# Kernel tuning notes

Measured on AMD Instinct MI355X. Metric: run time of the kernel, lower is better.

Reference implementation:

```python
import jax, jax.numpy as jnp
import numpy as np

B, S, E, H = 4, 2048, 1024, 16
D = E // H  # head dim = 64
NEG = -1e9


def setup_inputs() -> dict:
    key = jax.random.key(0)
    ks = jax.random.split(key, 6)
    scale = 1.0 / np.sqrt(E)
    return {
        "x": jax.random.normal(ks[0], (B, S, E), dtype=jnp.float32),
        "in_proj_weight": jax.random.normal(ks[1], (3 * E, E), dtype=jnp.float32) * scale,
        "in_proj_bias": jax.random.normal(ks[2], (3 * E,), dtype=jnp.float32) * 0.02,
        "out_proj_weight": jax.random.normal(ks[3], (E, E), dtype=jnp.float32) * scale,
        "out_proj_bias": jax.random.normal(ks[4], (E,), dtype=jnp.float32) * 0.02,
        "mask": jax.random.randint(ks[5], (B, S), 0, 2, dtype=jnp.int32),
    }


def reference(x, in_proj_weight, in_proj_bias, out_proj_weight, out_proj_bias, mask):
    # Equivalent of F.multi_head_attention_forward(h,h,h,...) with batch-first x.
    # qkv projection: [B,S,3E]
    qkv = jnp.einsum("bse,fe->bsf", x, in_proj_weight) + in_proj_bias
    q, k, v = jnp.split(qkv, 3, axis=-1)
    # split heads -> [B,S,H,D]
    q = q.reshape(B, S, H, D) * (1.0 / np.sqrt(D))
    k = k.reshape(B, S, H, D)
    v = v.reshape(B, S, H, D)
    # scores [B,H,Sq,Sk]
    scores = jnp.einsum("bqhd,bkhd->bhqk", q, k)
    # key_padding_mask = (mask == 0): True positions are excluded
    pad = (mask == 0)[:, None, None, :]  # [B,1,1,Sk]
    scores = jnp.where(pad, NEG, scores)
    attn = jax.nn.softmax(scores, axis=-1)
    # attention output -> [B,S,E]
    ctx = jnp.einsum("bhqk,bkhd->bqhd", attn, v).reshape(B, S, E)
    h_ = jnp.einsum("bse,fe->bsf", ctx, out_proj_weight) + out_proj_bias
    # residual; dropout is identity in eval mode
    return x + h_
```

## Files before the change

kernel.cpp:

```cpp
#include <hip/hip_runtime.h>
#include <stdint.h>
#include <math.h>

#define B_ 4
#define S_ 2048
#define E_ 1024
#define H_ 16
#define D_ 64
#define M_ (B_*S_)

typedef __attribute__((ext_vector_type(8))) short bf16x8;
typedef __attribute__((ext_vector_type(4))) float f32x4;

__device__ __forceinline__ unsigned short f2bf(float f) {
  union { float f; uint32_t u; } v; v.f = f;
  uint32_t u = v.u;
  return (unsigned short)((u + 0x7FFFu + ((u >> 16) & 1u)) >> 16);
}

__device__ __forceinline__ void gload16(const void* g, void* l) {
  __builtin_amdgcn_global_load_lds(
      (__attribute__((address_space(1))) void*)g,
      (__attribute__((address_space(3))) void*)l, 16, 0, 0);
}

__device__ __forceinline__ uint32_t cvtpk(float lo, float hi) {
  uint32_t r;
  asm("v_cvt_pk_bf16_f32 %0, %1, %2" : "=v"(r) : "v"(lo), "v"(hi));
  return r;
}

#define N1 ((M_*E_)/4)
#define N2 ((3*E_*E_)/4)
#define N3 ((E_*E_)/4)
#define NM ((B_*S_)/4)
__global__ __launch_bounds__(256) void cvt_all(const float* __restrict__ x,
                                               const float* __restrict__ w1,
                                               const float* __restrict__ w2,
                                               const int* __restrict__ mask,
                                               unsigned short* __restrict__ dst,
                                               float* __restrict__ maskf) {
  int i = blockIdx.x * 256 + threadIdx.x;
  if (i < N1 + N2 + N3) {
    const float* src;
    int j;
    if (i < N1) { src = x; j = i; }
    else if (i < N1 + N2) { src = w1; j = i - N1; }
    else { src = w2; j = i - N1 - N2; }
    float4 v = reinterpret_cast<const float4*>(src)[j];
    ushort4 o;
    o.x = f2bf(v.x); o.y = f2bf(v.y); o.z = f2bf(v.z); o.w = f2bf(v.w);
    reinterpret_cast<ushort4*>(dst)[i] = o;
  } else if (i < N1 + N2 + N3 + NM) {
    int j = i - (N1 + N2 + N3);
    int4 m = reinterpret_cast<const int4*>(mask)[j];
    float4 o;
    o.x = m.x ? 0.0f : -2.0e9f;
    o.y = m.y ? 0.0f : -2.0e9f;
    o.z = m.z ? 0.0f : -2.0e9f;
    o.w = m.w ? 0.0f : -2.0e9f;
    reinterpret_cast<float4*>(maskf)[j] = o;
  }
}

__device__ __forceinline__ void stage_half(const unsigned short* src,
                                           unsigned short* dst, int tid, int o0) {
  gload16(src + o0, dst + tid * 8);
  gload16(src + o0 + 65536, dst + tid * 8 + 4096);
}

template<int Q, int W>
__device__ __forceinline__ void phase256(
    const unsigned short* At, const unsigned short* Bt,
    bf16x8 (&bfm)[4][2], f32x4 (&acc)[8][4],
    const unsigned short* ssrc, unsigned short* sdst,
    int tid, int o0, int wm, int wn, int l15, int lg)
{
  bf16x8 afr[2][2];
  if constexpr (Q == 0) {
    const unsigned short* bh = Bt + (wn >> 1) * 8192;
    #pragma unroll
    for (int nf = 0; nf < 4; ++nf) {
      const int rowB = (wn & 1) * 64 + nf * 16 + l15;
      #pragma unroll
      for (int ks = 0; ks < 2; ++ks)
        bfm[nf][ks] = *(const bf16x8*)&bh[rowB * 64 + (((ks*4 + lg) ^ (rowB & 7)) * 8)];
    }
  }
  const unsigned short* ah = At + wm * 8192;
  #pragma unroll
  for (int sub = 0; sub < 2; ++sub) {
    const int rowA = (2*Q + sub) * 16 + l15;
    #pragma unroll
    for (int ks = 0; ks < 2; ++ks)
      afr[sub][ks] = *(const bf16x8*)&ah[rowA * 64 + (((ks*4 + lg) ^ (rowA & 7)) * 8)];
  }
  if (ssrc) stage_half(ssrc, sdst, tid, o0);
  if constexpr (W == 2) asm volatile("s_waitcnt vmcnt(2)" ::: "memory");
  if constexpr (W == 4) asm volatile("s_waitcnt vmcnt(4)" ::: "memory");
  if constexpr (W == 9) asm volatile("s_waitcnt vmcnt(0)" ::: "memory");
  asm volatile("" ::: "memory");
  __builtin_amdgcn_s_barrier();
  asm volatile("s_waitcnt lgkmcnt(0)" ::: "memory");
  __builtin_amdgcn_sched_barrier(0);
  __builtin_amdgcn_s_setprio(1);
  #pragma unroll
  for (int sub = 0; sub < 2; ++sub)
    #pragma unroll
    for (int nf = 0; nf < 4; ++nf)
      #pragma unroll
      for (int ks = 0; ks < 2; ++ks)
        acc[2*Q + sub][nf] = __builtin_amdgcn_mfma_f32_16x16x32_bf16(
            afr[sub][ks], bfm[nf][ks], acc[2*Q + sub][nf], 0, 0, 0);
  __builtin_amdgcn_s_setprio(0);
  asm volatile("" ::: "memory");
  __builtin_amdgcn_s_barrier();
  asm volatile("" ::: "memory");
}

__global__ __launch_bounds__(512, 2) void gemm_qkv8(
    const unsigned short* __restrict__ A,
    const unsigned short* __restrict__ W,
    const float* __restrict__ bias,
    unsigned short* __restrict__ Qg,
    unsigned short* __restrict__ Kg,
    unsigned short* __restrict__ Vtg)
{
  __shared__ __align__(16) unsigned short AsF[2 * 16384];
  __shared__ __align__(16) unsigned short BsF[2 * 16384];
  const int tid = threadIdx.x;
  const int lane = tid & 63, wave = tid >> 6;
  const int wm = wave >> 2, wn = wave & 3;
  const int l15 = lane & 15, lg = lane >> 4;

  int lin = blockIdx.y * 12 + blockIdx.x;
  lin = (lin & 7) * 48 + (lin >> 3);
  const int tm = (lin / 12) * 256;
  const int tn = (lin % 12) * 256;

  const int o0 = (tid >> 3) * 1024 + (((tid & 7) ^ ((tid >> 3) & 7)) * 8);
  const unsigned short* Ab = A + (size_t)tm * 1024;
  const unsigned short* Bb = W + (size_t)tn * 1024;

#define SRCA(t,h) (Ab + (size_t)((t)*64 + (h)*131072))
#define SRCB(t,h) (Bb + (size_t)((t)*64 + (h)*131072))
#define DSTA(b,h) (AsF + (b)*16384 + (h)*8192)
#define DSTB(b,h) (BsF + (b)*16384 + (h)*8192)

  f32x4 acc[8][4];
  #pragma unroll
  for (int mi = 0; mi < 8; ++mi)
    #pragma unroll
    for (int nf = 0; nf < 4; ++nf) acc[mi][nf] = (f32x4){0.f, 0.f, 0.f, 0.f};
  bf16x8 bfm[4][2];

  stage_half(SRCA(0,0), DSTA(0,0), tid, o0);
  stage_half(SRCA(0,1), DSTA(0,1), tid, o0);
  stage_half(SRCB(0,0), DSTB(0,0), tid, o0);
  stage_half(SRCB(0,1), DSTB(0,1), tid, o0);
  stage_half(SRCB(1,0), DSTB(1,0), tid, o0);
  stage_half(SRCB(1,1), DSTB(1,1), tid, o0);
  asm volatile("s_waitcnt vmcnt(4)" ::: "memory");
  __builtin_amdgcn_s_barrier();
  asm volatile("" ::: "memory");

  for (int i = 0; i < 7; ++i) {
    const int t2 = 2 * i;
    const unsigned short* A0t = DSTA(0,0);
    const unsigned short* B0t = DSTB(0,0);
    const unsigned short* A1t = DSTA(1,0);
    const unsigned short* B1t = DSTB(1,0);
    phase256<0,0>(A0t, B0t, bfm, acc, SRCA(t2+1,0), DSTA(1,0), tid, o0, wm, wn, l15, lg);
    phase256<1,0>(A0t, B0t, bfm, acc, SRCB(t2+2,0), DSTB(0,0), tid, o0, wm, wn, l15, lg);
    phase256<2,0>(A0t, B0t, bfm, acc, SRCB(t2+2,1), DSTB(0,1), tid, o0, wm, wn, l15, lg);
    phase256<3,0>(A0t, B0t, bfm, acc, SRCA(t2+1,1), DSTA(1,1), tid, o0, wm, wn, l15, lg);
    phase256<0,2>(A1t, B1t, bfm, acc, SRCA(t2+2,0), DSTA(0,0), tid, o0, wm, wn, l15, lg);
    phase256<1,0>(A1t, B1t, bfm, acc, SRCA(t2+2,1), DSTA(0,1), tid, o0, wm, wn, l15, lg);
    phase256<2,0>(A1t, B1t, bfm, acc, SRCB(t2+3,0), DSTB(1,0), tid, o0, wm, wn, l15, lg);
    phase256<3,4>(A1t, B1t, bfm, acc, SRCB(t2+3,1), DSTB(1,1), tid, o0, wm, wn, l15, lg);
  }
  {
    const unsigned short* A0t = DSTA(0,0);
    const unsigned short* B0t = DSTB(0,0);
    const unsigned short* A1t = DSTA(1,0);
    const unsigned short* B1t = DSTB(1,0);
    phase256<0,0>(A0t, B0t, bfm, acc, SRCA(15,0), DSTA(1,0), tid, o0, wm, wn, l15, lg);
    phase256<1,0>(A0t, B0t, bfm, acc, nullptr, nullptr, tid, o0, wm, wn, l15, lg);
    phase256<2,0>(A0t, B0t, bfm, acc, nullptr, nullptr, tid, o0, wm, wn, l15, lg);
    phase256<3,0>(A0t, B0t, bfm, acc, SRCA(15,1), DSTA(1,1), tid, o0, wm, wn, l15, lg);
    phase256<0,9>(A1t, B1t, bfm, acc, nullptr, nullptr, tid, o0, wm, wn, l15, lg);
    phase256<1,0>(A1t, B1t, bfm, acc, nullptr, nullptr, tid, o0, wm, wn, l15, lg);
    phase256<2,0>(A1t, B1t, bfm, acc, nullptr, nullptr, tid, o0, wm, wn, l15, lg);
    phase256<3,0>(A1t, B1t, bfm, acc, nullptr, nullptr, tid, o0, wm, wn, l15, lg);
  }
#undef SRCA
#undef SRCB
#undef DSTA
#undef DSTB

  #pragma unroll
  for (int nf = 0; nf < 4; ++nf) {
    const int col = tn + wn * 64 + nf * 16 + l15;
    const float bcol = bias[col];
    const int sec = col >> 10;
    const int f2 = col & 1023;
    const int h = f2 >> 6, d = f2 & 63;
    #pragma unroll
    for (int mi = 0; mi < 8; ++mi) {
      #pragma unroll
      for (int r = 0; r < 4; ++r) {
        const int row = tm + wm * 128 + mi * 16 + lg * 4 + r;
        const int b = row >> 11, s = row & (S_-1);
        const size_t bh = (size_t)(b * H_ + h);
        float val = acc[mi][nf][r] + bcol;
        if (sec == 0) {
          Qg[(bh*S_ + s)*D_ + d] = f2bf(val * 0.18033688f);
        } else if (sec == 1) {
          const int ch = (d >> 3) ^ (s & 7);
          Kg[(bh*S_ + s)*D_ + ch*8 + (d & 7)] = f2bf(val);
        } else {
          const int c2 = ((s >> 3) & 7) ^ (d & 7);
          Vtg[(bh*D_ + d)*S_ + (s & ~63) + c2*8 + (s & 7)] = f2bf(val);
        }
      }
    }
  }
}

__global__ __launch_bounds__(512, 4) void attn_fwd(
    const unsigned short* __restrict__ Qg,
    const unsigned short* __restrict__ Kg,
    const unsigned short* __restrict__ Vtg,
    const float* __restrict__ maskf,
    unsigned short* __restrict__ ctx)
{
  __shared__ __align__(16) unsigned short Ks[2][4096];
  __shared__ __align__(16) unsigned short Vs[2][4096];
  const int tid = threadIdx.x, lane = tid & 63, wave = tid >> 6;
  const int l15 = lane & 15, lg = lane >> 4;
  const int bh = blockIdx.y, b = bh >> 4, h = bh & 15;
  const int q0 = blockIdx.x * 256 + wave * 32;
  const unsigned short* Qb = Qg + (size_t)bh * S_ * D_;
  const unsigned short* Kb = Kg + (size_t)bh * S_ * D_;
  const unsigned short* Vb = Vtg + (size_t)bh * D_ * S_;
  const float* mrow = maskf + b * S_;

  bf16x8 qf[2][2];
  #pragma unroll
  for (int mi = 0; mi < 2; ++mi)
    #pragma unroll
    for (int kc = 0; kc < 2; ++kc)
      qf[mi][kc] = *(const bf16x8*)&Qb[(size_t)(q0 + mi*16 + l15)*D_ + kc*32 + lg*8];

  f32x4 zero4 = {0.f, 0.f, 0.f, 0.f};
  f32x4 accO[2][4];
  f32x4 accL[2] = {zero4, zero4};
  #pragma unroll
  for (int mi = 0; mi < 2; ++mi)
    #pragma unroll
    for (int df = 0; df < 4; ++df) accO[mi][df] = zero4;

  union { uint32_t u[4]; bf16x8 v; } ou;
  ou.u[0] = ou.u[1] = ou.u[2] = ou.u[3] = 0x3F803F80u;
  const bf16x8 onesv = ou.v;

  int kboff0[4], kboff1[4], vboff0[4], vboff1[4];
  #pragma unroll
  for (int kt = 0; kt < 4; ++kt) {
    const int krow = kt*16 + l15;
    kboff0[kt] = (krow*64 + ((lg ^ (krow & 7))*8)) * 2;
    kboff1[kt] = (krow*64 + (((4+lg) ^ (krow & 7))*8)) * 2;
  }
  #pragma unroll
  for (int df = 0; df < 4; ++df) {
    const int vrow = df*16 + l15;
    vboff0[df] = (vrow*64 + ((lg ^ (vrow & 7))*8)) * 2;
    vboff1[df] = (vrow*64 + (((4+lg) ^ (vrow & 7))*8)) * 2;
  }
  const char* KsB = (const char*)&Ks[0][0];
  const char* VsB = (const char*)&Vs[0][0];

  const int sr0 = tid >> 3, sc0 = (tid & 7) * 8;

  gload16(Kb + (size_t)sr0 * D_ + sc0, &Ks[0][tid*8]);
  gload16(Vb + (size_t)sr0 * S_ + sc0, &Vs[0][tid*8]);
  f32x4 mv0[4], mv1[4];
  #pragma unroll
  for (int kt = 0; kt < 4; ++kt)
    mv0[kt] = *(const f32x4*)&mrow[kt*16 + lg*4];
  const unsigned short* kpre = Kb + (size_t)(64 + sr0) * D_ + sc0;
  const unsigned short* vpre = Vb + (size_t)sr0 * S_ + 64 + sc0;
  const float* mpre = mrow + 64 + lg*4;
  __syncthreads();

#define ATTN_TILE(CUR, MVC, MVN, DO_PF)                                         \
  {                                                                             \
    if (DO_PF) {                                                                \
      gload16(kpre, &Ks[(CUR)^1][tid*8]);                                       \
      gload16(vpre, &Vs[(CUR)^1][tid*8]);                                       \
      kpre += 64*D_; vpre += 64;                                                \
      _Pragma("unroll")                                                         \
      for (int kt = 0; kt < 4; ++kt)                                            \
        MVN[kt] = *(const f32x4*)&mpre[kt*16];                                  \
      mpre += 64;                                                               \
    }                                                                           \
    f32x4 s_[2][4];                                                             \
    __builtin_amdgcn_s_setprio(1);                                              \
    _Pragma("unroll")                                                           \
    for (int kt = 0; kt < 4; ++kt) {                                            \
      bf16x8 kf0 = *(const bf16x8*)(KsB + (CUR)*8192 + kboff0[kt]);             \
      bf16x8 kf1 = *(const bf16x8*)(KsB + (CUR)*8192 + kboff1[kt]);             \
      s_[0][kt] = __builtin_amdgcn_mfma_f32_16x16x32_bf16(kf0, qf[0][0], MVC[kt], 0, 0, 0); \
      s_[0][kt] = __builtin_amdgcn_mfma_f32_16x16x32_bf16(kf1, qf[0][1], s_[0][kt], 0, 0, 0); \
      s_[1][kt] = __builtin_amdgcn_mfma_f32_16x16x32_bf16(kf0, qf[1][0], MVC[kt], 0, 0, 0); \
      s_[1][kt] = __builtin_amdgcn_mfma_f32_16x16x32_bf16(kf1, qf[1][1], s_[1][kt], 0, 0, 0); \
    }                                                                           \
    __builtin_amdgcn_s_setprio(0);                                              \
    _Pragma("unroll")                                                           \
    for (int mi = 0; mi < 2; ++mi)                                              \
      _Pragma("unroll")                                                         \
      for (int kt = 0; kt < 4; ++kt)                                            \
        _Pragma("unroll")                                                       \
        for (int r = 0; r < 4; ++r)                                             \
          s_[mi][kt][r] = __builtin_amdgcn_exp2f(s_[mi][kt][r]);                \
    bf16x8 pa[2][2];                                                            \
    _Pragma("unroll")                                                           \
    for (int mi = 0; mi < 2; ++mi) {                                            \
      _Pragma("unroll")                                                         \
      for (int kk = 0; kk < 2; ++kk) {                                          \
        uint32_t a0 = cvtpk(s_[mi][2*kk][0],   s_[mi][2*kk][1]);                \
        uint32_t c1 = cvtpk(s_[mi][2*kk][2],   s_[mi][2*kk][3]);                \
        uint32_t b0 = cvtpk(s_[mi][2*kk+1][0], s_[mi][2*kk+1][1]);              \
        uint32_t d1 = cvtpk(s_[mi][2*kk+1][2], s_[mi][2*kk+1][3]);              \
        asm("v_permlane32_swap_b32 %0, %1" : "+v"(a0), "+v"(b0));               \
        asm("v_permlane16_swap_b32 %0, %1" : "+v"(a0), "+v"(b0));               \
        asm("v_permlane32_swap_b32 %0, %1" : "+v"(c1), "+v"(d1));               \
        asm("v_permlane16_swap_b32 %0, %1" : "+v"(c1), "+v"(d1));               \
        union { bf16x8 v; uint32_t u[4]; } w;                                   \
        w.u[0] = a0; w.u[1] = c1; w.u[2] = b0; w.u[3] = d1;                     \
        pa[mi][kk] = w.v;                                                       \
      }                                                                         \
    }                                                                           \
    __builtin_amdgcn_s_setprio(1);                                              \
    accL[0] = __builtin_amdgcn_mfma_f32_16x16x32_bf16(pa[0][0], onesv, accL[0], 0, 0, 0); \
    accL[1] = __builtin_amdgcn_mfma_f32_16x16x32_bf16(pa[1][0], onesv, accL[1], 0, 0, 0); \
    _Pragma("unroll")                                                           \
    for (int df = 0; df < 4; ++df) {                                            \
      bf16x8 vf = *(const bf16x8*)(VsB + (CUR)*8192 + vboff0[df]);              \
      accO[0][df] = __builtin_amdgcn_mfma_f32_16x16x32_bf16(pa[0][0], vf, accO[0][df], 0, 0, 0); \
      accO[1][df] = __builtin_amdgcn_mfma_f32_16x16x32_bf16(pa[1][0], vf, accO[1][df], 0, 0, 0); \
    }                                                                           \
    accL[0] = __builtin_amdgcn_mfma_f32_16x16x32_bf16(pa[0][1], onesv, accL[0], 0, 0, 0); \
    accL[1] = __builtin_amdgcn_mfma_f32_16x16x32_bf16(pa[1][1], onesv, accL[1], 0, 0, 0); \
    _Pragma("unroll")                                                           \
    for (int df = 0; df < 4; ++df) {                                            \
      bf16x8 vf = *(const bf16x8*)(VsB + (CUR)*8192 + vboff1[df]);              \
      accO[0][df] = __builtin_amdgcn_mfma_f32_16x16x32_bf16(pa[0][1], vf, accO[0][df], 0, 0, 0); \
      accO[1][df] = __builtin_amdgcn_mfma_f32_16x16x32_bf16(pa[1][1], vf, accO[1][df], 0, 0, 0); \
    }                                                                           \
    __builtin_amdgcn_s_setprio(0);                                              \
    __syncthreads();                                                            \
  }

  for (int tt = 0; tt < 32; tt += 2) {
    ATTN_TILE(0, mv0, mv1, 1)
    ATTN_TILE(1, mv1, mv0, (tt < 30))
  }
#undef ATTN_TILE

  #pragma unroll
  for (int mi = 0; mi < 2; ++mi) {
    #pragma unroll
    for (int r = 0; r < 4; ++r) {
      const float iv = 1.0f / accL[mi][r];
      const int srow = q0 + mi*16 + lg*4 + r;
      #pragma unroll
      for (int df = 0; df < 4; ++df) {
        const int d = df*16 + l15;
        ctx[((size_t)b*S_ + srow)*E_ + h*D_ + d] = f2bf(accO[mi][df][r] * iv);
      }
    }
  }
}

__global__ __launch_bounds__(256) void gemm_out(
    const unsigned short* __restrict__ A,
    const unsigned short* __restrict__ W,
    const float* __restrict__ bias,
    const float* __restrict__ xres,
    float* __restrict__ out)
{
  __shared__ __align__(16) unsigned short As[128*32];
  __shared__ __align__(16) unsigned short Bs[128*32];
  const int tid = threadIdx.x;
  const int lane = tid & 63;
  const int wave = tid >> 6;
  const int wm = (wave >> 1) * 64, wn = (wave & 1) * 64;
  const int tm = blockIdx.y * 128, tn = blockIdx.x * 128;
  const int l15 = lane & 15, lg = lane >> 4;

  f32x4 zero4 = {0.f, 0.f, 0.f, 0.f};
  f32x4 acc[4][4];
  #pragma unroll
  for (int mi = 0; mi < 4; ++mi)
    #pragma unroll
    for (int ni = 0; ni < 4; ++ni) acc[mi][ni] = zero4;

  const int r0 = tid >> 2, c0 = (tid & 3) * 8;
  const unsigned short* Arow0 = A + (size_t)(tm + r0) * E_ + c0;
  const unsigned short* Arow1 = A + (size_t)(tm + r0 + 64) * E_ + c0;
  const unsigned short* Wrow0 = W + (size_t)(tn + r0) * E_ + c0;
  const unsigned short* Wrow1 = W + (size_t)(tn + r0 + 64) * E_ + c0;
  unsigned short* lA0 = As + tid * 8;
  unsigned short* lA1 = As + (tid + 256) * 8;
  unsigned short* lB0 = Bs + tid * 8;
  unsigned short* lB1 = Bs + (tid + 256) * 8;

  for (int k0 = 0; k0 < E_; k0 += 32) {
    gload16(Arow0 + k0, lA0);
    gload16(Arow1 + k0, lA1);
    gload16(Wrow0 + k0, lB0);
    gload16(Wrow1 + k0, lB1);
    __syncthreads();
    bf16x8 af[4], bfm[4];
    #pragma unroll
    for (int mi = 0; mi < 4; ++mi)
      af[mi] = *(const bf16x8*)&As[(wm + mi*16 + l15)*32 + lg*8];
    #pragma unroll
    for (int ni = 0; ni < 4; ++ni)
      bfm[ni] = *(const bf16x8*)&Bs[(wn + ni*16 + l15)*32 + lg*8];
    #pragma unroll
    for (int mi = 0; mi < 4; ++mi)
      #pragma unroll
      for (int ni = 0; ni < 4; ++ni)
        acc[mi][ni] = __builtin_amdgcn_mfma_f32_16x16x32_bf16(af[mi], bfm[ni], acc[mi][ni], 0, 0, 0);
    __syncthreads();
  }

  #pragma unroll
  for (int ni = 0; ni < 4; ++ni) {
    const int col = tn + wn + ni*16 + l15;
    const float bcol = bias[col];
    #pragma unroll
    for (int mi = 0; mi < 4; ++mi) {
      #pragma unroll
      for (int r = 0; r < 4; ++r) {
        const int row = tm + wm + mi*16 + lg*4 + r;
        out[(size_t)row*E_ + col] = xres[(size_t)row*E_ + col] + acc[mi][ni][r] + bcol;
      }
    }
  }
}

extern "C" void kernel_launch(void* const* d_in, const int* in_sizes, int n_in,
                              void* d_out, int out_size, void* d_ws, size_t ws_size,
                              hipStream_t stream) {
  const float* x  = (const float*)d_in[0];
  const float* w1 = (const float*)d_in[1];
  const float* b1 = (const float*)d_in[2];
  const float* w2 = (const float*)d_in[3];
  const float* b2 = (const float*)d_in[4];
  const int* mask = (const int*)d_in[5];
  float* out = (float*)d_out;

  const size_t SZ = (size_t)B_*H_*S_*D_;
  unsigned short* Qg  = (unsigned short*)d_ws;
  unsigned short* Kg  = Qg + SZ;
  unsigned short* Vtg = Kg + SZ;
  unsigned short* xb  = Vtg + SZ;
  unsigned short* w1b = xb + (size_t)M_*E_;
  unsigned short* w2b = w1b + (size_t)3*E_*E_;
  float* maskf = (float*)(w2b + (size_t)E_*E_);
  unsigned short* ctx = xb;

  const int ntot = N1 + N2 + N3 + NM;
  cvt_all<<<(ntot + 255)/256, 256, 0, stream>>>(x, w1, w2, mask, xb, maskf);

  gemm_qkv8<<<dim3(12, 32), 512, 0, stream>>>(xb, w1b, b1, Qg, Kg, Vtg);
  attn_fwd<<<dim3(S_/256, B_*H_), 512, 0, stream>>>(Qg, Kg, Vtg, maskf, ctx);
  gemm_out<<<dim3(E_/128, M_/128), 256, 0, stream>>>(ctx, w2b, b2, x, out);
}
```

Baseline: 231.0 us.

## Replace pipelined 256x256 QKV GEMM with simple 128x128 tile and LDS-transposed V store

Swaps the double-buffered, phase-scheduled 256x256 QKV projection kernel for a simpler 128x128 tile kernel. The new kernel uses 256 threads, a 32-wide K step and two __syncthreads per iteration, and remaps blocks so each XCD works on contiguous column tiles. The V section now goes through an LDS transpose so it can write the transposed, swizzled V with 16-byte coalesced stores instead of scattered 2-byte stores. The intent is more blocks for occupancy and better V store efficiency. In exchange it loses the load/compute overlap, the LDS swizzle and the larger per-block reuse, so the GEMM may become latency bound with bank conflicts.

```diff
diff --git a/kernel.cpp b/kernel.cpp
--- a/kernel.cpp
+++ b/kernel.cpp
@@ -63,62 +63,7 @@
   }
 }
 
-__device__ __forceinline__ void stage_half(const unsigned short* src,
-                                           unsigned short* dst, int tid, int o0) {
-  gload16(src + o0, dst + tid * 8);
-  gload16(src + o0 + 65536, dst + tid * 8 + 4096);
-}
-
-template<int Q, int W>
-__device__ __forceinline__ void phase256(
-    const unsigned short* At, const unsigned short* Bt,
-    bf16x8 (&bfm)[4][2], f32x4 (&acc)[8][4],
-    const unsigned short* ssrc, unsigned short* sdst,
-    int tid, int o0, int wm, int wn, int l15, int lg)
-{
-  bf16x8 afr[2][2];
-  if constexpr (Q == 0) {
-    const unsigned short* bh = Bt + (wn >> 1) * 8192;
-    #pragma unroll
-    for (int nf = 0; nf < 4; ++nf) {
-      const int rowB = (wn & 1) * 64 + nf * 16 + l15;
-      #pragma unroll
-      for (int ks = 0; ks < 2; ++ks)
-        bfm[nf][ks] = *(const bf16x8*)&bh[rowB * 64 + (((ks*4 + lg) ^ (rowB & 7)) * 8)];
-    }
-  }
-  const unsigned short* ah = At + wm * 8192;
-  #pragma unroll
-  for (int sub = 0; sub < 2; ++sub) {
-    const int rowA = (2*Q + sub) * 16 + l15;
-    #pragma unroll
-    for (int ks = 0; ks < 2; ++ks)
-      afr[sub][ks] = *(const bf16x8*)&ah[rowA * 64 + (((ks*4 + lg) ^ (rowA & 7)) * 8)];
-  }
-  if (ssrc) stage_half(ssrc, sdst, tid, o0);
-  if constexpr (W == 2) asm volatile("s_waitcnt vmcnt(2)" ::: "memory");
-  if constexpr (W == 4) asm volatile("s_waitcnt vmcnt(4)" ::: "memory");
-  if constexpr (W == 9) asm volatile("s_waitcnt vmcnt(0)" ::: "memory");
-  asm volatile("" ::: "memory");
-  __builtin_amdgcn_s_barrier();
-  asm volatile("s_waitcnt lgkmcnt(0)" ::: "memory");
-  __builtin_amdgcn_sched_barrier(0);
-  __builtin_amdgcn_s_setprio(1);
-  #pragma unroll
-  for (int sub = 0; sub < 2; ++sub)
-    #pragma unroll
-    for (int nf = 0; nf < 4; ++nf)
-      #pragma unroll
-      for (int ks = 0; ks < 2; ++ks)
-        acc[2*Q + sub][nf] = __builtin_amdgcn_mfma_f32_16x16x32_bf16(
-            afr[sub][ks], bfm[nf][ks], acc[2*Q + sub][nf], 0, 0, 0);
-  __builtin_amdgcn_s_setprio(0);
-  asm volatile("" ::: "memory");
-  __builtin_amdgcn_s_barrier();
-  asm volatile("" ::: "memory");
-}
-
-__global__ __launch_bounds__(512, 2) void gemm_qkv8(
+__global__ __launch_bounds__(256) void gemm_qkv128(
     const unsigned short* __restrict__ A,
     const unsigned short* __restrict__ W,
     const float* __restrict__ bias,
@@ -126,103 +71,113 @@
     unsigned short* __restrict__ Kg,
     unsigned short* __restrict__ Vtg)
 {
-  __shared__ __align__(16) unsigned short AsF[2 * 16384];
-  __shared__ __align__(16) unsigned short BsF[2 * 16384];
+  __shared__ __align__(16) unsigned short SMEM[128*136];
+  unsigned short* As = SMEM;
+  unsigned short* Bs = SMEM + 4096;
   const int tid = threadIdx.x;
-  const int lane = tid & 63, wave = tid >> 6;
-  const int wm = wave >> 2, wn = wave & 3;
+  const int lane = tid & 63;
+  const int wave = tid >> 6;
+  const int wm = (wave >> 1) * 64, wn = (wave & 1) * 64;
   const int l15 = lane & 15, lg = lane >> 4;
 
-  int lin = blockIdx.y * 12 + blockIdx.x;
-  lin = (lin & 7) * 48 + (lin >> 3);
-  const int tm = (lin / 12) * 256;
-  const int tn = (lin % 12) * 256;
-
-  const int o0 = (tid >> 3) * 1024 + (((tid & 7) ^ ((tid >> 3) & 7)) * 8);
-  const unsigned short* Ab = A + (size_t)tm * 1024;
-  const unsigned short* Bb = W + (size_t)tn * 1024;
-
-#define SRCA(t,h) (Ab + (size_t)((t)*64 + (h)*131072))
-#define SRCB(t,h) (Bb + (size_t)((t)*64 + (h)*131072))
-#define DSTA(b,h) (AsF + (b)*16384 + (h)*8192)
-#define DSTB(b,h) (BsF + (b)*16384 + (h)*8192)
-
-  f32x4 acc[8][4];
-  #pragma unroll
-  for (int mi = 0; mi < 8; ++mi)
-    #pragma unroll
-    for (int nf = 0; nf < 4; ++nf) acc[mi][nf] = (f32x4){0.f, 0.f, 0.f, 0.f};
-  bf16x8 bfm[4][2];
-
-  stage_half(SRCA(0,0), DSTA(0,0), tid, o0);
-  stage_half(SRCA(0,1), DSTA(0,1), tid, o0);
-  stage_half(SRCB(0,0), DSTB(0,0), tid, o0);
-  stage_half(SRCB(0,1), DSTB(0,1), tid, o0);
-  stage_half(SRCB(1,0), DSTB(1,0), tid, o0);
-  stage_half(SRCB(1,1), DSTB(1,1), tid, o0);
-  asm volatile("s_waitcnt vmcnt(4)" ::: "memory");
-  __builtin_amdgcn_s_barrier();
-  asm volatile("" ::: "memory");
-
-  for (int i = 0; i < 7; ++i) {
-    const int t2 = 2 * i;
-    const unsigned short* A0t = DSTA(0,0);
-    const unsigned short* B0t = DSTB(0,0);
-    const unsigned short* A1t = DSTA(1,0);
-    const unsigned short* B1t = DSTB(1,0);
-    phase256<0,0>(A0t, B0t, bfm, acc, SRCA(t2+1,0), DSTA(1,0), tid, o0, wm, wn, l15, lg);
-    phase256<1,0>(A0t, B0t, bfm, acc, SRCB(t2+2,0), DSTB(0,0), tid, o0, wm, wn, l15, lg);
-    phase256<2,0>(A0t, B0t, bfm, acc, SRCB(t2+2,1), DSTB(0,1), tid, o0, wm, wn, l15, lg);
-    phase256<3,0>(A0t, B0t, bfm, acc, SRCA(t2+1,1), DSTA(1,1), tid, o0, wm, wn, l15, lg);
-    phase256<0,2>(A1t, B1t, bfm, acc, SRCA(t2+2,0), DSTA(0,0), tid, o0, wm, wn, l15, lg);
-    phase256<1,0>(A1t, B1t, bfm, acc, SRCA(t2+2,1), DSTA(0,1), tid, o0, wm, wn, l15, lg);
-    phase256<2,0>(A1t, B1t, bfm, acc, SRCB(t2+3,0), DSTB(1,0), tid, o0, wm, wn, l15, lg);
-    phase256<3,4>(A1t, B1t, bfm, acc, SRCB(t2+3,1), DSTB(1,1), tid, o0, wm, wn, l15, lg);
-  }
-  {
-    const unsigned short* A0t = DSTA(0,0);
-    const unsigned short* B0t = DSTB(0,0);
-    const unsigned short* A1t = DSTA(1,0);
-    const unsigned short* B1t = DSTB(1,0);
-    phase256<0,0>(A0t, B0t, bfm, acc, SRCA(15,0), DSTA(1,0), tid, o0, wm, wn, l15, lg);
-    phase256<1,0>(A0t, B0t, bfm, acc, nullptr, nullptr, tid, o0, wm, wn, l15, lg);
-    phase256<2,0>(A0t, B0t, bfm, acc, nullptr, nullptr, tid, o0, wm, wn, l15, lg);
-    phase256<3,0>(A0t, B0t, bfm, acc, SRCA(15,1), DSTA(1,1), tid, o0, wm, wn, l15, lg);
-    phase256<0,9>(A1t, B1t, bfm, acc, nullptr, nullptr, tid, o0, wm, wn, l15, lg);
-    phase256<1,0>(A1t, B1t, bfm, acc, nullptr, nullptr, tid, o0, wm, wn, l15, lg);
-    phase256<2,0>(A1t, B1t, bfm, acc, nullptr, nullptr, tid, o0, wm, wn, l15, lg);
-    phase256<3,0>(A1t, B1t, bfm, acc, nullptr, nullptr, tid, o0, wm, wn, l15, lg);
-  }
-#undef SRCA
-#undef SRCB
-#undef DSTA
-#undef DSTB
-
-  #pragma unroll
-  for (int nf = 0; nf < 4; ++nf) {
-    const int col = tn + wn * 64 + nf * 16 + l15;
-    const float bcol = bias[col];
-    const int sec = col >> 10;
-    const int f2 = col & 1023;
-    const int h = f2 >> 6, d = f2 & 63;
-    #pragma unroll
-    for (int mi = 0; mi < 8; ++mi) {
-      #pragma unroll
-      for (int r = 0; r < 4; ++r) {
-        const int row = tm + wm * 128 + mi * 16 + lg * 4 + r;
-        const int b = row >> 11, s = row & (S_-1);
-        const size_t bh = (size_t)(b * H_ + h);
-        float val = acc[mi][nf][r] + bcol;
-        if (sec == 0) {
-          Qg[(bh*S_ + s)*D_ + d] = f2bf(val * 0.18033688f);
-        } else if (sec == 1) {
-          const int ch = (d >> 3) ^ (s & 7);
-          Kg[(bh*S_ + s)*D_ + ch*8 + (d & 7)] = f2bf(val);
-        } else {
-          const int c2 = ((s >> 3) & 7) ^ (d & 7);
-          Vtg[(bh*D_ + d)*S_ + (s & ~63) + c2*8 + (s & 7)] = f2bf(val);
+  const int orig = blockIdx.y * 24 + blockIdx.x;
+  const int xcd = orig & 7;
+  const int idx = orig >> 3;
+  const int tn = (xcd * 3 + (idx % 3)) * 128;
+  const int tm = (idx / 3) * 128;
+
+  f32x4 zero4 = {0.f, 0.f, 0.f, 0.f};
+  f32x4 acc[4][4];
+  #pragma unroll
+  for (int mi = 0; mi < 4; ++mi)
+    #pragma unroll
+    for (int ni = 0; ni < 4; ++ni) acc[mi][ni] = zero4;
+
+  const int r0 = tid >> 2, c0 = (tid & 3) * 8;
+  const unsigned short* Arow0 = A + (size_t)(tm + r0) * E_ + c0;
+  const unsigned short* Arow1 = A + (size_t)(tm + r0 + 64) * E_ + c0;
+  const unsigned short* Wrow0 = W + (size_t)(tn + r0) * E_ + c0;
+  const unsigned short* Wrow1 = W + (size_t)(tn + r0 + 64) * E_ + c0;
+  unsigned short* lA0 = As + tid * 8;
+  unsigned short* lA1 = As + (tid + 256) * 8;
+  unsigned short* lB0 = Bs + tid * 8;
+  unsigned short* lB1 = Bs + (tid + 256) * 8;
+
+  for (int k0 = 0; k0 < E_; k0 += 32) {
+    gload16(Arow0 + k0, lA0);
+    gload16(Arow1 + k0, lA1);
+    gload16(Wrow0 + k0, lB0);
+    gload16(Wrow1 + k0, lB1);
+    __syncthreads();
+    bf16x8 af[4], bfm[4];
+    #pragma unroll
+    for (int mi = 0; mi < 4; ++mi)
+      af[mi] = *(const bf16x8*)&As[(wm + mi*16 + l15)*32 + lg*8];
+    #pragma unroll
+    for (int ni = 0; ni < 4; ++ni)
+      bfm[ni] = *(const bf16x8*)&Bs[(wn + ni*16 + l15)*32 + lg*8];
+    #pragma unroll
+    for (int mi = 0; mi < 4; ++mi)
+      #pragma unroll
+      for (int ni = 0; ni < 4; ++ni)
+        acc[mi][ni] = __builtin_amdgcn_mfma_f32_16x16x32_bf16(af[mi], bfm[ni], acc[mi][ni], 0, 0, 0);
+    __syncthreads();
+  }
+
+  const int sec = tn >> 10;
+  if (sec < 2) {
+    #pragma unroll
+    for (int ni = 0; ni < 4; ++ni) {
+      const int col = tn + wn + ni*16 + l15;
+      const float bcol = bias[col];
+      const int f2 = col & 1023;
+      const int h = f2 >> 6, d = f2 & 63;
+      #pragma unroll
+      for (int mi = 0; mi < 4; ++mi) {
+        #pragma unroll
+        for (int r = 0; r < 4; ++r) {
+          const int row = tm + wm + mi*16 + lg*4 + r;
+          const int b = row >> 11, s = row & (S_-1);
+          const size_t bh = (size_t)(b * H_ + h);
+          float val = acc[mi][ni][r] + bcol;
+          if (sec == 0) {
+            Qg[(bh*S_ + s)*D_ + d] = f2bf(val * 0.18033688f);
+          } else {
+            const int ch = (d >> 3) ^ (s & 7);
+            Kg[(bh*S_ + s)*D_ + ch*8 + (d & 7)] = f2bf(val);
+          }
         }
       }
+    }
+  } else {
+    __syncthreads();
+    unsigned short* T = SMEM;
+    #pragma unroll
+    for (int ni = 0; ni < 4; ++ni) {
+      const int f = wn + ni*16 + l15;
+      const float bcol = bias[tn + f];
+      #pragma unroll
+      for (int mi = 0; mi < 4; ++mi) {
+        const int s0 = wm + mi*16 + lg*4;
+        uint2 p;
+        p.x = cvtpk(acc[mi][ni][0] + bcol, acc[mi][ni][1] + bcol);
+        p.y = cvtpk(acc[mi][ni][2] + bcol, acc[mi][ni][3] + bcol);
+        *reinterpret_cast<uint2*>(&T[f*136 + s0]) = p;
+      }
+    }
+    __syncthreads();
+    const int f = tid >> 1, sch = tid & 1;
+    const int d = f & 63, hl = f >> 6;
+    const int h = ((tn & 1023) >> 6) + hl;
+    const int b = tm >> 11;
+    const size_t bh = (size_t)(b * H_ + h);
+    const int sbase = (tm & (S_-1)) + sch*64;
+    unsigned short* vout = Vtg + (bh*D_ + d)*S_ + sbase;
+    const unsigned short* tin = &T[f*136 + sch*64];
+    #pragma unroll
+    for (int j = 0; j < 8; ++j) {
+      uint4 v = *reinterpret_cast<const uint4*>(&tin[j*8]);
+      *reinterpret_cast<uint4*>(&vout[(j ^ (d & 7))*8]) = v;
     }
   }
 }
@@ -476,7 +431,7 @@
   const int ntot = N1 + N2 + N3 + NM;
   cvt_all<<<(ntot + 255)/256, 256, 0, stream>>>(x, w1, w2, mask, xb, maskf);
 
-  gemm_qkv8<<<dim3(12, 32), 512, 0, stream>>>(xb, w1b, b1, Qg, Kg, Vtg);
+  gemm_qkv128<<<dim3(24, 64), 256, 0, stream>>>(xb, w1b, b1, Qg, Kg, Vtg);
   attn_fwd<<<dim3(S_/256, B_*H_), 512, 0, stream>>>(Qg, Kg, Vtg, maskf, ctx);
   gemm_out<<<dim3(E_/128, M_/128), 256, 0, stream>>>(ctx, w2b, b2, x, out);
 }
```

Result: faster. 226.4 us (-2.0%).
